# Optimization experiments

Hardware: AMD Instinct MI355X
Metric: run time of the kernel (lower is better)

The kernel has to match this reference:

```python
import jax, jax.numpy as jnp
import numpy as np

H = 1024        # bridge_hidden_dim
NH = 16         # num_attention_heads
HD = H // NH    # head_dim = 64
B, S = 4, 1024
PHYS_W = 0.2
CONS_W = 0.15


def setup_inputs() -> dict:
    key = jax.random.key(0)
    ks = jax.random.split(key, 16)
    sc = 0.02
    return {
        "cnn_features": jax.random.normal(ks[0], (B, S, H), jnp.float32),
        "llm_features": jax.random.normal(ks[1], (B, S, H), jnp.float32),
        "Wq": jax.random.normal(ks[2], (H, H), jnp.float32) * sc,
        "bq": jnp.zeros((H,), jnp.float32),
        "Wk": jax.random.normal(ks[3], (H, H), jnp.float32) * sc,
        "bk": jnp.zeros((H,), jnp.float32),
        "Wv": jax.random.normal(ks[4], (H, H), jnp.float32) * sc,
        "bv": jnp.zeros((H,), jnp.float32),
        "Wo": jax.random.normal(ks[5], (H, H), jnp.float32) * sc,
        "bo": jnp.zeros((H,), jnp.float32),
        "ln_g": jnp.ones((H,), jnp.float32),
        "ln_b": jnp.zeros((H,), jnp.float32),
        "e_energy": jax.random.normal(ks[6], (H,), jnp.float32),
        "e_mass": jax.random.normal(ks[7], (H,), jnp.float32),
        "e_momentum": jax.random.normal(ks[8], (H,), jnp.float32),
    }


def _layernorm(x, g, b, eps=1e-5):
    mu = jnp.mean(x, axis=-1, keepdims=True)
    var = jnp.var(x, axis=-1, keepdims=True)
    return (x - mu) * jax.lax.rsqrt(var + eps) * g + b


def _split_heads(x):
    b, s, _ = x.shape
    return x.reshape(b, s, NH, HD).transpose(0, 2, 1, 3)  # [b, h, s, d]


def _physics_attention(q_in, k_in, v_in, Wq, bq, Wk, bk, Wv, bv, Wo, bo, ln_g, ln_b):
    # q_in: [b, sq, H]; k_in == v_in: [b, sk, H] with sq == sk (required by bias math)
    Q = _split_heads(q_in @ Wq.T + bq)  # [b,h,s,d]
    K = _split_heads(k_in @ Wk.T + bk)
    V = _split_heads(v_in @ Wv.T + bv)
    scores = jnp.einsum('bhqd,bhkd->bhqk', Q, K) / jnp.sqrt(jnp.float32(HD))
    # physics constraints (broadcast [b,h,s,1] over key axis)
    energy_bias = jnp.sum(Q * K, axis=-1, keepdims=True) * PHYS_W
    mass_bias = jnp.mean(Q + K, axis=-1, keepdims=True) * CONS_W
    scores = scores + energy_bias + mass_bias
    attn = jax.nn.softmax(scores, axis=-1)  # dropout is identity in eval
    att = jnp.einsum('bhqk,bhkd->bhqd', attn, V)
    b, h, s, d = att.shape
    att = att.transpose(0, 2, 1, 3).reshape(b, s, h * d)
    out = att @ Wo.T + bo
    return _layernorm(q_in + out, ln_g, ln_b)


def reference(cnn_features, llm_features, Wq, bq, Wk, bk, Wv, bv, Wo, bo,
              ln_g, ln_b, e_energy, e_mass, e_momentum):
    b = cnn_features.shape[0]
    phys = jnp.stack([e_energy, e_mass, e_momentum], axis=0)  # [3, H]
    phys = jnp.broadcast_to(phys[None], (b, 3, H))
    aug_cnn = jnp.concatenate([cnn_features, phys], axis=1)  # [b, S+3, H]
    aug_llm = jnp.concatenate([llm_features, phys], axis=1)
    cnn_att = _physics_attention(aug_cnn, aug_llm, aug_llm,
                                 Wq, bq, Wk, bk, Wv, bv, Wo, bo, ln_g, ln_b)
    llm_att = _physics_attention(aug_llm, aug_cnn, aug_cnn,
                                 Wq, bq, Wk, bk, Wv, bv, Wo, bo, ln_g, ln_b)
    cnn_out = cnn_att[:, :cnn_features.shape[1], :]
    llm_out = llm_att[:, :llm_features.shape[1], :]
    return (cnn_out, llm_out)
```

## Files before the change

### kernel.cpp

```cpp
#include <hip/hip_runtime.h>
#include <stdint.h>

#define SA 1027
#define SPAD 1088

typedef __attribute__((ext_vector_type(8))) short short8;
typedef __attribute__((ext_vector_type(4))) float f32x4;
typedef __attribute__((ext_vector_type(2))) unsigned int u32x2;

typedef const __attribute__((address_space(1))) uint8_t* gas1;
typedef __attribute__((address_space(3))) uint8_t* las3;

__device__ __forceinline__ void gload16(const void* g, void* l){
  __builtin_amdgcn_global_load_lds((gas1)g, (las3)l, 16, 0, 0);
}

__device__ __forceinline__ uint16_t f2bf(float f){
  uint32_t x = __builtin_bit_cast(uint32_t, f);
  x = (x + 0x7fffu + ((x >> 16) & 1u)) >> 16;
  return (uint16_t)x;
}
__device__ __forceinline__ float bf2f(uint16_t u){
  uint32_t x = ((uint32_t)u) << 16;
  return __builtin_bit_cast(float, x);
}

__device__ __forceinline__ f32x4 mfma16(short8 a, short8 b, f32x4 c){
  return __builtin_amdgcn_mfma_f32_16x16x32_bf16(a, b, c, 0, 0, 0);
}

#define QSCALE 0.18033688011112042f

__global__ __launch_bounds__(256) void prep_all(
    const float* __restrict__ cnn, const float* __restrict__ llm,
    const float* __restrict__ Wq, const float* __restrict__ Wk,
    const float* __restrict__ Wv, const float* __restrict__ Wo,
    const float* __restrict__ bq, const float* __restrict__ bk,
    const float* __restrict__ bv, const float* __restrict__ bo,
    const float* __restrict__ ee, const float* __restrict__ em,
    const float* __restrict__ ep,
    uint16_t* __restrict__ W, float* __restrict__ bias,
    uint16_t* __restrict__ X, uint16_t* __restrict__ Yqk,
    uint16_t* __restrict__ Vt){
  const int bid = blockIdx.x;
  if (bid < 4100){
    const int gid = bid*256 + threadIdx.x;
    if (gid < 1048576){
      const int w = gid >> 18;
      const int off = (gid & 262143) << 2;
      const float* src = (w==0) ? Wq : (w==1) ? Wk : (w==2) ? Wv : Wo;
      const float4 v = *(const float4*)(src + off);
      ushort4 u;
      u.x = f2bf(v.x); u.y = f2bf(v.y); u.z = f2bf(v.z); u.w = f2bf(v.w);
      *(ushort4*)(W + ((size_t)w << 20) + off) = u;
    } else if (gid < 1048576 + 1024){
      const int i = (gid - 1048576) << 2;
      const int w = i >> 10;
      const int off = i & 1023;
      const float* src = (w==0) ? bq : (w==1) ? bk : (w==2) ? bv : bo;
      *(float4*)(bias + i) = *(const float4*)(src + off);
    }
  } else if (bid < 8196){
    const int rb = bid - 4100;
    const int row = rb*2 + (threadIdx.x >> 7);
    const int c8 = (threadIdx.x & 127) << 3;
    const int cb = row >> 10, s = row & 1023;
    const int c = cb >> 2, b = cb & 3;
    const float* src = (c ? llm : cnn) + ((size_t)(b*1024 + s))*1024 + c8;
    const float4 v0 = *(const float4*)src;
    const float4 v1 = *(const float4*)(src + 4);
    short8 u;
    u[0]=(short)f2bf(v0.x); u[1]=(short)f2bf(v0.y); u[2]=(short)f2bf(v0.z); u[3]=(short)f2bf(v0.w);
    u[4]=(short)f2bf(v1.x); u[5]=(short)f2bf(v1.y); u[6]=(short)f2bf(v1.z); u[7]=(short)f2bf(v1.w);
    *(short8*)(X + (size_t)row*1024 + c8) = u;
  } else {
    __shared__ float xs[1024];
    const int pb = bid - 8196;
    const int t = pb >> 3;
    const int col = 1024 + (pb & 7)*256 + threadIdx.x;
    const float* e = (t==0) ? ee : (t==1) ? em : ep;
    for (int k = threadIdx.x; k < 1024; k += 256) xs[k] = bf2f(f2bf(e[k]));
    __syncthreads();
    const float* wrow = (col < 2048) ? (Wk + (size_t)(col-1024)*1024)
                                     : (Wv + (size_t)(col-2048)*1024);
    const float bb = (col < 2048) ? bk[col-1024] : bv[col-2048];
    float acc = 0.f;
    for (int k = 0; k < 1024; k += 4){
      const float4 w4 = *(const float4*)(wrow + k);
      acc += bf2f(f2bf(w4.x))*xs[k] + bf2f(f2bf(w4.y))*xs[k+1]
           + bf2f(f2bf(w4.z))*xs[k+2] + bf2f(f2bf(w4.w))*xs[k+3];
    }
    const uint16_t o = f2bf(acc + bb);
    if (col < 2048){
      #pragma unroll
      for (int cb = 0; cb < 8; ++cb)
        Yqk[((size_t)cb*SA + 1024 + t)*2048 + col] = o;
    } else {
      const int hd = col - 2048;
      #pragma unroll
      for (int cb = 0; cb < 8; ++cb)
        Vt[((size_t)(cb*1024 + hd))*SPAD + 1024 + t] = o;
    }
  }
}

__global__ __launch_bounds__(512, 4) void qkv128(
    const uint16_t* __restrict__ A, const uint16_t* __restrict__ B,
    const float* __restrict__ bias, uint16_t* __restrict__ Yqk,
    uint16_t* __restrict__ Vt){
  extern __shared__ uint8_t lds[];
  const int tid = threadIdx.x;
  const int lane = tid & 63, wid = tid >> 6;
  const int l15 = lane & 15, l4 = lane >> 4;
  const int wm = wid >> 2, wn = wid & 3;
  const int wg = (blockIdx.x & 7)*128 + (blockIdx.x >> 3);
  const int bm = wg >> 4, bn = wg & 15;

  const uint16_t* Ag = A + (size_t)bm*128*1024;
  const uint16_t* Bg = B + (size_t)bn*192*1024;

  const int srow8 = lane >> 3;
  const int gch = (lane & 7) ^ srow8;
  const int c0 = wid*2, c1 = c0 + 1;
  const size_t ga0 = (size_t)(c0*8 + srow8)*1024 + gch*8;
  const size_t ga1 = (size_t)(c1*8 + srow8)*1024 + gch*8;
  const size_t gb0 = (size_t)((wid*3+0)*8 + srow8)*1024 + gch*8;
  const size_t gb1 = (size_t)((wid*3+1)*8 + srow8)*1024 + gch*8;
  const size_t gb2 = (size_t)((wid*3+2)*8 + srow8)*1024 + gch*8;

#define STG_A(buf, kt) do { \
    gload16(Ag + (size_t)(kt)*64 + ga0, lds + (buf)*40960 + c0*1024); \
    gload16(Ag + (size_t)(kt)*64 + ga1, lds + (buf)*40960 + c1*1024); \
  } while(0)
#define STG_B(buf, kt) do { \
    gload16(Bg + (size_t)(kt)*64 + gb0, lds + (buf)*40960 + 16384 + (wid*3+0)*1024); \
    gload16(Bg + (size_t)(kt)*64 + gb1, lds + (buf)*40960 + 16384 + (wid*3+1)*1024); \
    gload16(Bg + (size_t)(kt)*64 + gb2, lds + (buf)*40960 + 16384 + (wid*3+2)*1024); \
  } while(0)

  int koff[2];
  koff[0] = (l4*16) ^ ((l15 & 7) << 4);
  koff[1] = (64 + l4*16) ^ ((l15 & 7) << 4);
  const int arow = (wm*64 + l15) * 128;
  const int bbase = 16384 + (wn*48 + l15) * 128;

  f32x4 acc[4][3];
  #pragma unroll
  for (int i = 0; i < 4; ++i)
    #pragma unroll
    for (int j = 0; j < 3; ++j) acc[i][j] = (f32x4){0.f,0.f,0.f,0.f};

  const int NT = 16;
  STG_A(0,0); STG_B(0,0); STG_B(1,1);
  asm volatile("s_waitcnt vmcnt(3)" ::: "memory");
  __builtin_amdgcn_s_barrier();

  for (int s = 0; s < NT; ++s){
    const int b = s & 1, nb = b ^ 1;
    const uint8_t* L = lds + b*40960;
    short8 af[2][2], af2[2][2], bfr[3][2];

    if (s+1 < NT){ STG_A(nb, s+1); }
    #pragma unroll
    for (int i = 0; i < 2; ++i){
      af[i][0] = *(const short8*)(L + arow + i*2048 + koff[0]);
      af[i][1] = *(const short8*)(L + arow + i*2048 + koff[1]);
    }
    #pragma unroll
    for (int j = 0; j < 3; ++j){
      bfr[j][0] = *(const short8*)(L + bbase + j*2048 + koff[0]);
      bfr[j][1] = *(const short8*)(L + bbase + j*2048 + koff[1]);
    }
    __builtin_amdgcn_s_barrier();
    asm volatile("s_waitcnt lgkmcnt(0)" ::: "memory");
    __builtin_amdgcn_s_setprio(1);
    #pragma unroll
    for (int i = 0; i < 2; ++i)
      #pragma unroll
      for (int j = 0; j < 3; ++j)
        acc[i][j] = mfma16(af[i][1], bfr[j][1], mfma16(af[i][0], bfr[j][0], acc[i][j]));
    __builtin_amdgcn_s_setprio(0);
    __builtin_amdgcn_s_barrier();

    if (s+2 < NT){ STG_B(b, s+2); }
    #pragma unroll
    for (int i = 0; i < 2; ++i){
      af2[i][0] = *(const short8*)(L + arow + 4096 + i*2048 + koff[0]);
      af2[i][1] = *(const short8*)(L + arow + 4096 + i*2048 + koff[1]);
    }
    __builtin_amdgcn_s_barrier();
    asm volatile("s_waitcnt lgkmcnt(0)" ::: "memory");
    __builtin_amdgcn_s_setprio(1);
    #pragma unroll
    for (int i = 0; i < 2; ++i)
      #pragma unroll
      for (int j = 0; j < 3; ++j)
        acc[i+2][j] = mfma16(af2[i][1], bfr[j][1], mfma16(af2[i][0], bfr[j][0], acc[i+2][j]));
    __builtin_amdgcn_s_setprio(0);
    if (s < NT-2)       asm volatile("s_waitcnt vmcnt(3)" ::: "memory");
    else if (s == NT-2) asm volatile("s_waitcnt vmcnt(0)" ::: "memory");
    __builtin_amdgcn_s_barrier();
  }

  #pragma unroll
  for (int j = 0; j < 3; ++j){
    const int n = bn*192 + wn*48 + j*16 + l15;
    const float bb = bias[n];
    if (n < 2048){
      const float sc = (n < 1024) ? QSCALE : 1.0f;
      #pragma unroll
      for (int i = 0; i < 4; ++i){
        const int m0 = bm*128 + wm*64 + i*16 + l4*4;
        #pragma unroll
        for (int r = 0; r < 4; ++r){
          const int m = m0 + r;
          Yqk[((size_t)(m >> 10)*SA + (m & 1023))*2048 + n] = f2bf((acc[i][j][r] + bb) * sc);
        }
      }
    } else {
      const int hd = n - 2048;
      #pragma unroll
      for (int i = 0; i < 4; ++i){
        const int m0 = bm*128 + wm*64 + i*16 + l4*4;
        const size_t vrow = (size_t)(m0 >> 10)*1024 + hd;
        const uint32_t w0 = (uint32_t)f2bf(acc[i][j][0] + bb) | ((uint32_t)f2bf(acc[i][j][1] + bb) << 16);
        const uint32_t w1 = (uint32_t)f2bf(acc[i][j][2] + bb) | ((uint32_t)f2bf(acc[i][j][3] + bb) << 16);
        *(u32x2*)(Vt + vrow*SPAD + (m0 & 1023)) = (u32x2){w0, w1};
      }
    }
  }
#undef STG_A
#undef STG_B
}

__global__ __launch_bounds__(512, 4) void oproj128(
    const uint16_t* __restrict__ A, const uint16_t* __restrict__ B,
    const float* __restrict__ bias, uint16_t* __restrict__ C){
  extern __shared__ uint8_t lds[];
  const int tid = threadIdx.x;
  const int lane = tid & 63, wid = tid >> 6;
  const int l15 = lane & 15, l4 = lane >> 4;
  const int wm = wid >> 2, wn = wid & 3;
  const int wg = (blockIdx.x & 7)*64 + (blockIdx.x >> 3);
  const int bm = wg >> 3, bn = wg & 7;

  const uint16_t* Ag = A + (size_t)bm*128*1024;
  const uint16_t* Bg = B + (size_t)bn*128*1024;

  const int srow8 = lane >> 3;
  const int gch = (lane & 7) ^ srow8;
  const int c0 = wid*2, c1 = c0 + 1;
  const size_t ga0 = (size_t)(c0*8 + srow8)*1024 + gch*8;
  const size_t ga1 = (size_t)(c1*8 + srow8)*1024 + gch*8;

#define STG_A(buf, kt) do { \
    gload16(Ag + (size_t)(kt)*64 + ga0, lds + (buf)*32768 + c0*1024); \
    gload16(Ag + (size_t)(kt)*64 + ga1, lds + (buf)*32768 + c1*1024); \
  } while(0)
#define STG_B(buf, kt) do { \
    gload16(Bg + (size_t)(kt)*64 + ga0, lds + (buf)*32768 + 16384 + c0*1024); \
    gload16(Bg + (size_t)(kt)*64 + ga1, lds + (buf)*32768 + 16384 + c1*1024); \
  } while(0)

  int koff[2];
  koff[0] = (l4*16) ^ ((l15 & 7) << 4);
  koff[1] = (64 + l4*16) ^ ((l15 & 7) << 4);
  const int arow = (wm*64 + l15) * 128;
  const int bbase = 16384 + (wn*32 + l15) * 128;

  f32x4 acc[4][2];
  #pragma unroll
  for (int i = 0; i < 4; ++i){ acc[i][0] = (f32x4){0,0,0,0}; acc[i][1] = (f32x4){0,0,0,0}; }

  const int NT = 16;
  STG_A(0,0); STG_B(0,0); STG_B(1,1);
  asm volatile("s_waitcnt vmcnt(2)" ::: "memory");
  __builtin_amdgcn_s_barrier();

  for (int s = 0; s < NT; ++s){
    const int b = s & 1, nb = b ^ 1;
    const uint8_t* L = lds + b*32768;
    short8 af[2][2], af2[2][2], bfr[2][2];

    if (s+1 < NT){ STG_A(nb, s+1); }
    #pragma unroll
    for (int i = 0; i < 2; ++i){
      af[i][0] = *(const short8*)(L + arow + i*2048 + koff[0]);
      af[i][1] = *(const short8*)(L + arow + i*2048 + koff[1]);
    }
    #pragma unroll
    for (int j = 0; j < 2; ++j){
      bfr[j][0] = *(const short8*)(L + bbase + j*2048 + koff[0]);
      bfr[j][1] = *(const short8*)(L + bbase + j*2048 + koff[1]);
    }
    __builtin_amdgcn_s_barrier();
    asm volatile("s_waitcnt lgkmcnt(0)" ::: "memory");
    __builtin_amdgcn_s_setprio(1);
    #pragma unroll
    for (int i = 0; i < 2; ++i)
      #pragma unroll
      for (int j = 0; j < 2; ++j)
        acc[i][j] = mfma16(af[i][1], bfr[j][1], mfma16(af[i][0], bfr[j][0], acc[i][j]));
    __builtin_amdgcn_s_setprio(0);
    __builtin_amdgcn_s_barrier();

    if (s+2 < NT){ STG_B(b, s+2); }
    #pragma unroll
    for (int i = 0; i < 2; ++i){
      af2[i][0] = *(const short8*)(L + arow + 4096 + i*2048 + koff[0]);
      af2[i][1] = *(const short8*)(L + arow + 4096 + i*2048 + koff[1]);
    }
    __builtin_amdgcn_s_barrier();
    asm volatile("s_waitcnt lgkmcnt(0)" ::: "memory");
    __builtin_amdgcn_s_setprio(1);
    #pragma unroll
    for (int i = 0; i < 2; ++i)
      #pragma unroll
      for (int j = 0; j < 2; ++j)
        acc[i+2][j] = mfma16(af2[i][1], bfr[j][1], mfma16(af2[i][0], bfr[j][0], acc[i+2][j]));
    __builtin_amdgcn_s_setprio(0);
    if (s < NT-2)       asm volatile("s_waitcnt vmcnt(2)" ::: "memory");
    else if (s == NT-2) asm volatile("s_waitcnt vmcnt(0)" ::: "memory");
    __builtin_amdgcn_s_barrier();
  }

  #pragma unroll
  for (int j = 0; j < 2; ++j){
    const int n = bn*128 + wn*32 + j*16 + l15;
    const float bb = bias[n];
    #pragma unroll
    for (int i = 0; i < 4; ++i){
      const size_t m0 = (size_t)bm*128 + wm*64 + i*16 + l4*4;
      #pragma unroll
      for (int r = 0; r < 4; ++r)
        C[(m0 + r)*1024 + n] = f2bf(acc[i][j][r] + bb);
    }
  }
#undef STG_A
#undef STG_B
}

__global__ __launch_bounds__(512, 4) void attn_k(
    const uint16_t* __restrict__ Yqk, const uint16_t* __restrict__ Vt,
    uint16_t* __restrict__ att){
  extern __shared__ uint8_t lds[];
  const int tid = threadIdx.x;
  const int lane = tid & 63, wid = tid >> 6;
  const int l15 = lane & 15, l4 = lane >> 4;
  const int i = blockIdx.x;
  const int inst = (i & 7)*16 + ((i >> 3) & 15);
  const int qb = i >> 7;
  const int h = inst & 15, cb = inst >> 4;
  const size_t yrow0 = (size_t)cb * SA;
  const int q0 = qb*256 + wid*32;
  const size_t vbase = (size_t)inst * 64 * SPAD;
  const uint16_t* Yk = Yqk + yrow0*2048 + 1024 + h*64;

  short8 qf[2][2];
  #pragma unroll
  for (int u = 0; u < 2; ++u){
    const uint16_t* p = Yqk + (yrow0 + q0 + u*16 + l15)*2048 + h*64 + l4*8;
    qf[u][0] = *(const short8*)p;
    qf[u][1] = *(const short8*)(p + 32);
  }

  f32x4 o0[4], o1[4];
  float psum0 = 0.f, psum1 = 0.f;
  #pragma unroll
  for (int d = 0; d < 4; ++d){ o0[d] = (f32x4){0,0,0,0}; o1[d] = (f32x4){0,0,0,0}; }

  int koff[2], koffp[2], pwo[4];
  #pragma unroll
  for (int kk = 0; kk < 2; ++kk){
    koff[kk]  = (l15*128 + kk*64 + l4*16) ^ ((l15 & 7) << 4);
    koffp[kk] = l15*144 + kk*64 + l4*16;
  }
  #pragma unroll
  for (int nt = 0; nt < 4; ++nt)
    pwo[nt] = l15*144 + nt*32 + l4*8;
  uint8_t* const pb = lds + 49152 + wid*2304;

  const int srow = lane >> 3, schunk = lane & 7;
  const int strow = wid*8 + srow;
  const int sgch = schunk ^ srow;

#define ASTAGE(t3, kt) do { \
    gload16(Yk + (size_t)((kt)*64 + strow)*2048 + sgch*8, lds + (t3)*8192 + wid*1024); \
    gload16(Vt + vbase + (size_t)strow*SPAD + (kt)*64 + sgch*8, lds + 24576 + (t3)*8192 + wid*1024); \
  } while(0)

  ASTAGE(0, 0);
  ASTAGE(1, 1);
  asm volatile("s_waitcnt vmcnt(2)" ::: "memory");
  __builtin_amdgcn_s_barrier();

  for (int kt = 0; kt < 17; ++kt){
    const int c3 = kt % 3;
    if (kt <= 14){ const int t3 = (kt + 2) % 3; ASTAGE(t3, kt + 2); }
    const uint8_t* bK = lds + c3*8192;
    const uint8_t* bV = lds + 24576 + c3*8192;

    f32x4 sa[4], sb[4];
    #pragma unroll
    for (int nt = 0; nt < 4; ++nt){
      const short8 k0 = *(const short8*)(bK + nt*2048 + koff[0]);
      const short8 k1 = *(const short8*)(bK + nt*2048 + koff[1]);
      sa[nt] = mfma16(k1, qf[0][1], mfma16(k0, qf[0][0], (f32x4){0,0,0,0}));
      sb[nt] = mfma16(k1, qf[1][1], mfma16(k0, qf[1][0], (f32x4){0,0,0,0}));
    }
    if (kt == 16){
      #pragma unroll
      for (int nt = 0; nt < 4; ++nt)
        #pragma unroll
        for (int r = 0; r < 4; ++r){
          if (nt*16 + l4*4 + r >= 3){ sa[nt][r] = -3e38f; sb[nt][r] = -3e38f; }
        }
    }
    #pragma unroll
    for (int nt = 0; nt < 4; ++nt){
      const float p0 = __builtin_amdgcn_exp2f(sa[nt][0]);
      const float p1 = __builtin_amdgcn_exp2f(sa[nt][1]);
      const float p2 = __builtin_amdgcn_exp2f(sa[nt][2]);
      const float p3 = __builtin_amdgcn_exp2f(sa[nt][3]);
      psum0 += (p0 + p1) + (p2 + p3);
      uint32_t w0, w1;
      asm("v_cvt_pk_bf16_f32 %0, %1, %2" : "=v"(w0) : "v"(p0), "v"(p1));
      asm("v_cvt_pk_bf16_f32 %0, %1, %2" : "=v"(w1) : "v"(p2), "v"(p3));
      *(u32x2*)(pb + pwo[nt]) = (u32x2){w0, w1};
    }
    short8 vf[4][2];
    #pragma unroll
    for (int dt = 0; dt < 4; ++dt){
      vf[dt][0] = *(const short8*)(bV + dt*2048 + koff[0]);
      vf[dt][1] = *(const short8*)(bV + dt*2048 + koff[1]);
    }
    #pragma unroll
    for (int kk = 0; kk < 2; ++kk){
      const short8 pf = *(const short8*)(pb + koffp[kk]);
      #pragma unroll
      for (int dt = 0; dt < 4; ++dt)
        o0[dt] = mfma16(pf, vf[dt][kk], o0[dt]);
    }
    #pragma unroll
    for (int nt = 0; nt < 4; ++nt){
      const float p0 = __builtin_amdgcn_exp2f(sb[nt][0]);
      const float p1 = __builtin_amdgcn_exp2f(sb[nt][1]);
      const float p2 = __builtin_amdgcn_exp2f(sb[nt][2]);
      const float p3 = __builtin_amdgcn_exp2f(sb[nt][3]);
      psum1 += (p0 + p1) + (p2 + p3);
      uint32_t w0, w1;
      asm("v_cvt_pk_bf16_f32 %0, %1, %2" : "=v"(w0) : "v"(p0), "v"(p1));
      asm("v_cvt_pk_bf16_f32 %0, %1, %2" : "=v"(w1) : "v"(p2), "v"(p3));
      *(u32x2*)(pb + pwo[nt]) = (u32x2){w0, w1};
    }
    #pragma unroll
    for (int kk = 0; kk < 2; ++kk){
      const short8 pf = *(const short8*)(pb + koffp[kk]);
      #pragma unroll
      for (int dt = 0; dt < 4; ++dt)
        o1[dt] = mfma16(pf, vf[dt][kk], o1[dt]);
    }
    if (kt <= 14)      asm volatile("s_waitcnt vmcnt(2)" ::: "memory");
    else if (kt == 15) asm volatile("s_waitcnt vmcnt(0)" ::: "memory");
    if (kt <= 15) __builtin_amdgcn_s_barrier();
  }
#undef ASTAGE

  psum0 += __shfl_xor(psum0, 16); psum0 += __shfl_xor(psum0, 32);
  psum1 += __shfl_xor(psum1, 16); psum1 += __shfl_xor(psum1, 32);
  const size_t arow0 = (size_t)cb*1024 + q0;
  #pragma unroll
  for (int r = 0; r < 4; ++r){
    const float inv0 = 1.f / __shfl(psum0, l4*4 + r);
    const float inv1 = 1.f / __shfl(psum1, l4*4 + r);
    #pragma unroll
    for (int dt = 0; dt < 4; ++dt){
      att[(arow0 + l4*4 + r)*1024 + h*64 + dt*16 + l15] = f2bf(o0[dt][r] * inv0);
      att[(arow0 + 16 + l4*4 + r)*1024 + h*64 + dt*16 + l15] = f2bf(o1[dt][r] * inv1);
    }
  }
}

__global__ __launch_bounds__(256) void ln_out(
    const uint16_t* __restrict__ Op, const float* __restrict__ cnn,
    const float* __restrict__ llm, const float* __restrict__ g,
    const float* __restrict__ b, float* __restrict__ out){
  const int row = blockIdx.x;
  const int c = row >> 12, bq = row & 4095;
  const int tid = threadIdx.x;
  const ushort4 u = *(const ushort4*)(Op + (size_t)row*1024 + (tid<<2));
  const float4 rv = *(const float4*)((c ? llm : cnn) + (size_t)bq*1024 + (tid<<2));
  const float x0 = bf2f(u.x) + rv.x;
  const float x1 = bf2f(u.y) + rv.y;
  const float x2 = bf2f(u.z) + rv.z;
  const float x3 = bf2f(u.w) + rv.w;
  float s1 = x0+x1+x2+x3;
  float s2 = x0*x0+x1*x1+x2*x2+x3*x3;
  #pragma unroll
  for (int m=1;m<64;m<<=1){ s1 += __shfl_xor(s1,m); s2 += __shfl_xor(s2,m); }
  __shared__ float r1[4], r2[4];
  const int wid = tid >> 6, lane = tid & 63;
  if (lane == 0){ r1[wid] = s1; r2[wid] = s2; }
  __syncthreads();
  s1 = r1[0]+r1[1]+r1[2]+r1[3];
  s2 = r2[0]+r2[1]+r2[2]+r2[3];
  const float mu = s1 * 0.0009765625f;
  const float var = s2 * 0.0009765625f - mu*mu;
  const float rs = rsqrtf(var + 1e-5f);
  const float4 gv = *(const float4*)(g + (tid<<2));
  const float4 bv = *(const float4*)(b + (tid<<2));
  float4 ov;
  ov.x = (x0 - mu)*rs*gv.x + bv.x;
  ov.y = (x1 - mu)*rs*gv.y + bv.y;
  ov.z = (x2 - mu)*rs*gv.z + bv.z;
  ov.w = (x3 - mu)*rs*gv.w + bv.w;
  *(float4*)(out + ((size_t)c << 22) + (size_t)bq*1024 + (tid<<2)) = ov;
}

extern "C" void kernel_launch(void* const* d_in, const int* in_sizes, int n_in,
                              void* d_out, int out_size, void* d_ws, size_t ws_size,
                              hipStream_t stream){
  const float* cnn = (const float*)d_in[0];
  const float* llm = (const float*)d_in[1];
  const float* Wq  = (const float*)d_in[2];
  const float* bq  = (const float*)d_in[3];
  const float* Wk  = (const float*)d_in[4];
  const float* bk  = (const float*)d_in[5];
  const float* Wv  = (const float*)d_in[6];
  const float* bv  = (const float*)d_in[7];
  const float* Wo  = (const float*)d_in[8];
  const float* bo  = (const float*)d_in[9];
  const float* lng = (const float*)d_in[10];
  const float* lnb = (const float*)d_in[11];
  const float* ee  = (const float*)d_in[12];
  const float* em  = (const float*)d_in[13];
  const float* ep  = (const float*)d_in[14];

  uint8_t* ws = (uint8_t*)d_ws;
  uint16_t* X    = (uint16_t*)(ws + 0);
  uint16_t* W    = (uint16_t*)(ws + 16777216);
  float*    bias = (float*)   (ws + 25165824);
  uint16_t* Yqk  = (uint16_t*)(ws + 25182208);
  uint16_t* Vt   = (uint16_t*)(ws + 59785216);
  uint16_t* att  = X;
  uint16_t* Op   = Yqk;
  float* out = (float*)d_out;

  hipFuncSetAttribute((const void*)qkv128,
                      hipFuncAttributeMaxDynamicSharedMemorySize, 81920);
  hipFuncSetAttribute((const void*)oproj128,
                      hipFuncAttributeMaxDynamicSharedMemorySize, 65536);
  hipFuncSetAttribute((const void*)attn_k,
                      hipFuncAttributeMaxDynamicSharedMemorySize, 67584);

  prep_all<<<8220, 256, 0, stream>>>(cnn, llm, Wq, Wk, Wv, Wo, bq, bk, bv, bo,
                                     ee, em, ep, W, bias, X, Yqk, Vt);
  qkv128<<<1024, 512, 81920, stream>>>(X, W, bias, Yqk, Vt);
  attn_k<<<512, 512, 67584, stream>>>(Yqk, Vt, att);
  oproj128<<<512, 512, 65536, stream>>>(att, W + 3145728, bias + 3072, Op);
  ln_out<<<8192, 256, 0, stream>>>(Op, cnn, llm, lng, lnb, out);
}
```

Measured before the change: 180.3 us.

## Enlarge output-projection GEMM tile to 256 rows and remap QKV block order

The output-projection GEMM now computes a 256x128 tile per workgroup, with 8 accumulator tiles per wave and a larger LDS double-buffer. The launch drops to 256 blocks and occupancy is lowered to 2 blocks per SIMD. The A-tile load is split across the two half-iterations. Separately, the QKV kernel's block-to-tile mapping is changed so each XCD covers a grouped band of row tiles, interleaving pairs, which is meant to improve L2 reuse. The larger tile cuts B-matrix refetches but reduces the number of blocks and occupancy on a 256-CU device.

```diff
diff --git a/kernel.cpp b/kernel.cpp
--- a/kernel.cpp
+++ b/kernel.cpp
@@ -113,8 +113,10 @@
   const int lane = tid & 63, wid = tid >> 6;
   const int l15 = lane & 15, l4 = lane >> 4;
   const int wm = wid >> 2, wn = wid & 3;
-  const int wg = (blockIdx.x & 7)*128 + (blockIdx.x >> 3);
-  const int bm = wg >> 4, bn = wg & 15;
+  const int xcd = blockIdx.x & 7, loc = blockIdx.x >> 3;
+  const int sb = loc >> 5, pos = loc & 31;
+  const int bm = xcd*8 + sb*2 + (pos & 1);
+  const int bn = pos >> 1;
 
   const uint16_t* Ag = A + (size_t)bm*128*1024;
   const uint16_t* Bg = B + (size_t)bn*192*1024;
@@ -233,7 +235,7 @@
 #undef STG_B
 }
 
-__global__ __launch_bounds__(512, 4) void oproj128(
+__global__ __launch_bounds__(512, 2) void oproj256(
     const uint16_t* __restrict__ A, const uint16_t* __restrict__ B,
     const float* __restrict__ bias, uint16_t* __restrict__ C){
   extern __shared__ uint8_t lds[];
@@ -241,10 +243,10 @@
   const int lane = tid & 63, wid = tid >> 6;
   const int l15 = lane & 15, l4 = lane >> 4;
   const int wm = wid >> 2, wn = wid & 3;
-  const int wg = (blockIdx.x & 7)*64 + (blockIdx.x >> 3);
+  const int wg = (blockIdx.x & 7)*32 + (blockIdx.x >> 3);
   const int bm = wg >> 3, bn = wg & 7;
 
-  const uint16_t* Ag = A + (size_t)bm*128*1024;
+  const uint16_t* Ag = A + (size_t)bm*256*1024;
   const uint16_t* Bg = B + (size_t)bn*128*1024;
 
   const int srow8 = lane >> 3;
@@ -253,40 +255,40 @@
   const size_t ga0 = (size_t)(c0*8 + srow8)*1024 + gch*8;
   const size_t ga1 = (size_t)(c1*8 + srow8)*1024 + gch*8;
 
-#define STG_A(buf, kt) do { \
-    gload16(Ag + (size_t)(kt)*64 + ga0, lds + (buf)*32768 + c0*1024); \
-    gload16(Ag + (size_t)(kt)*64 + ga1, lds + (buf)*32768 + c1*1024); \
+#define STG_A(buf, H, kt) do { \
+    gload16(Ag + (size_t)(H)*131072 + (size_t)(kt)*64 + ga0, lds + (buf)*49152 + (H)*16384 + c0*1024); \
+    gload16(Ag + (size_t)(H)*131072 + (size_t)(kt)*64 + ga1, lds + (buf)*49152 + (H)*16384 + c1*1024); \
   } while(0)
 #define STG_B(buf, kt) do { \
-    gload16(Bg + (size_t)(kt)*64 + ga0, lds + (buf)*32768 + 16384 + c0*1024); \
-    gload16(Bg + (size_t)(kt)*64 + ga1, lds + (buf)*32768 + 16384 + c1*1024); \
+    gload16(Bg + (size_t)(kt)*64 + ga0, lds + (buf)*49152 + 32768 + c0*1024); \
+    gload16(Bg + (size_t)(kt)*64 + ga1, lds + (buf)*49152 + 32768 + c1*1024); \
   } while(0)
 
   int koff[2];
   koff[0] = (l4*16) ^ ((l15 & 7) << 4);
   koff[1] = (64 + l4*16) ^ ((l15 & 7) << 4);
-  const int arow = (wm*64 + l15) * 128;
-  const int bbase = 16384 + (wn*32 + l15) * 128;
-
-  f32x4 acc[4][2];
-  #pragma unroll
-  for (int i = 0; i < 4; ++i){ acc[i][0] = (f32x4){0,0,0,0}; acc[i][1] = (f32x4){0,0,0,0}; }
+  const int abase = wm*16384 + l15*128;
+  const int bbase = 32768 + (wn*32 + l15)*128;
+
+  f32x4 acc[8][2];
+  #pragma unroll
+  for (int i = 0; i < 8; ++i){ acc[i][0] = (f32x4){0,0,0,0}; acc[i][1] = (f32x4){0,0,0,0}; }
 
   const int NT = 16;
-  STG_A(0,0); STG_B(0,0); STG_B(1,1);
+  STG_A(0,0,0); STG_A(0,1,0); STG_B(0,0); STG_B(1,1);
   asm volatile("s_waitcnt vmcnt(2)" ::: "memory");
   __builtin_amdgcn_s_barrier();
 
   for (int s = 0; s < NT; ++s){
     const int b = s & 1, nb = b ^ 1;
-    const uint8_t* L = lds + b*32768;
-    short8 af[2][2], af2[2][2], bfr[2][2];
-
-    if (s+1 < NT){ STG_A(nb, s+1); }
-    #pragma unroll
-    for (int i = 0; i < 2; ++i){
-      af[i][0] = *(const short8*)(L + arow + i*2048 + koff[0]);
-      af[i][1] = *(const short8*)(L + arow + i*2048 + koff[1]);
+    const uint8_t* L = lds + b*49152;
+    short8 af[4][2], af2[4][2], bfr[2][2];
+
+    if (s+1 < NT){ STG_A(nb, 0, s+1); }
+    #pragma unroll
+    for (int i = 0; i < 4; ++i){
+      af[i][0] = *(const short8*)(L + abase + i*2048 + koff[0]);
+      af[i][1] = *(const short8*)(L + abase + i*2048 + koff[1]);
     }
     #pragma unroll
     for (int j = 0; j < 2; ++j){
@@ -297,27 +299,28 @@
     asm volatile("s_waitcnt lgkmcnt(0)" ::: "memory");
     __builtin_amdgcn_s_setprio(1);
     #pragma unroll
-    for (int i = 0; i < 2; ++i)
+    for (int i = 0; i < 4; ++i)
       #pragma unroll
       for (int j = 0; j < 2; ++j)
         acc[i][j] = mfma16(af[i][1], bfr[j][1], mfma16(af[i][0], bfr[j][0], acc[i][j]));
     __builtin_amdgcn_s_setprio(0);
     __builtin_amdgcn_s_barrier();
 
+    if (s+1 < NT){ STG_A(nb, 1, s+1); }
     if (s+2 < NT){ STG_B(b, s+2); }
     #pragma unroll
-    for (int i = 0; i < 2; ++i){
-      af2[i][0] = *(const short8*)(L + arow + 4096 + i*2048 + koff[0]);
-      af2[i][1] = *(const short8*)(L + arow + 4096 + i*2048 + koff[1]);
+    for (int i = 0; i < 4; ++i){
+      af2[i][0] = *(const short8*)(L + abase + 8192 + i*2048 + koff[0]);
+      af2[i][1] = *(const short8*)(L + abase + 8192 + i*2048 + koff[1]);
     }
     __builtin_amdgcn_s_barrier();
     asm volatile("s_waitcnt lgkmcnt(0)" ::: "memory");
     __builtin_amdgcn_s_setprio(1);
     #pragma unroll
-    for (int i = 0; i < 2; ++i)
+    for (int i = 0; i < 4; ++i)
       #pragma unroll
       for (int j = 0; j < 2; ++j)
-        acc[i+2][j] = mfma16(af2[i][1], bfr[j][1], mfma16(af2[i][0], bfr[j][0], acc[i+2][j]));
+        acc[i+4][j] = mfma16(af2[i][1], bfr[j][1], mfma16(af2[i][0], bfr[j][0], acc[i+4][j]));
     __builtin_amdgcn_s_setprio(0);
     if (s < NT-2)       asm volatile("s_waitcnt vmcnt(2)" ::: "memory");
     else if (s == NT-2) asm volatile("s_waitcnt vmcnt(0)" ::: "memory");
@@ -329,8 +332,8 @@
     const int n = bn*128 + wn*32 + j*16 + l15;
     const float bb = bias[n];
     #pragma unroll
-    for (int i = 0; i < 4; ++i){
-      const size_t m0 = (size_t)bm*128 + wm*64 + i*16 + l4*4;
+    for (int i = 0; i < 8; ++i){
+      const size_t m0 = (size_t)bm*256 + wm*128 + i*16 + l4*4;
       #pragma unroll
       for (int r = 0; r < 4; ++r)
         C[(m0 + r)*1024 + n] = f2bf(acc[i][j][r] + bb);
@@ -548,8 +551,8 @@
 
   hipFuncSetAttribute((const void*)qkv128,
                       hipFuncAttributeMaxDynamicSharedMemorySize, 81920);
-  hipFuncSetAttribute((const void*)oproj128,
-                      hipFuncAttributeMaxDynamicSharedMemorySize, 65536);
+  hipFuncSetAttribute((const void*)oproj256,
+                      hipFuncAttributeMaxDynamicSharedMemorySize, 98304);
   hipFuncSetAttribute((const void*)attn_k,
                       hipFuncAttributeMaxDynamicSharedMemorySize, 67584);
 
@@ -557,6 +560,6 @@
                                      ee, em, ep, W, bias, X, Yqk, Vt);
   qkv128<<<1024, 512, 81920, stream>>>(X, W, bias, Yqk, Vt);
   attn_k<<<512, 512, 67584, stream>>>(Yqk, Vt, att);
-  oproj128<<<512, 512, 65536, stream>>>(att, W + 3145728, bias + 3072, Op);
+  oproj256<<<256, 512, 98304, stream>>>(att, W + 3145728, bias + 3072, Op);
   ln_out<<<8192, 256, 0, stream>>>(Op, cnn, llm, lng, lnb, out);
 }
```

New measurement: 183.0 us. No clear change (+1.5%).
